# Optimization experiments

Measured on AMD Instinct MI355X. Metric: run time of the kernel, lower is better.

Reference implementation:

```python
import jax, jax.numpy as jnp
import numpy as np

TOP_K = 2

def setup_inputs() -> dict:
    key = jax.random.key(0)
    k1, k2, k3, k4 = jax.random.split(key, 4)
    B, T, C, E = 4, 2048, 1024, 8
    x = jax.random.normal(k1, (B, T, C), dtype=jnp.float32)
    Wg = jax.random.normal(k2, (C, E), dtype=jnp.float32) * 0.02
    W1 = jax.random.normal(k3, (E, C, 4 * C), dtype=jnp.float32) * 0.02
    W2 = jax.random.normal(k4, (E, 4 * C, C), dtype=jnp.float32) * 0.02
    return {"x": x, "Wg": Wg, "W1": W1, "W2": W2}

def reference(x, Wg, W1, W2):
    B, T, C = x.shape
    E = W1.shape[0]
    xf = x.reshape(-1, C)                                   # [N, C]
    N = xf.shape[0]
    gate = jax.nn.softmax(xf @ Wg, axis=-1)                 # [N, E]
    top_w, top_i = jax.lax.top_k(gate, TOP_K)               # [N, k]
    top_w = top_w / (top_w.sum(axis=-1, keepdims=True) + 1e-9)
    # Dense all-expert compute (equivalent math to gather/MLP/scatter loop)
    h = jnp.maximum(jnp.einsum('nc,ecf->nef', xf, W1), 0.0)  # [N, E, 4C]
    y = jnp.einsum('nef,efc->nec', h, W2)                    # [N, E, C]
    # Scatter top-k weights into a dense [N, E] combine matrix
    comb = jnp.zeros((N, E), dtype=xf.dtype).at[jnp.arange(N)[:, None], top_i].add(top_w)
    out = jnp.einsum('nec,ne->nc', y, comb)                  # [N, C]
    return out.reshape(B, T, C)
```

## Files before the change

kernel.cpp:

```cpp
#include <hip/hip_runtime.h>
#include <hip/hip_bf16.h>
#include <hip/hip_fp16.h>


#define N_TOK 8192
#define C_DIM 1024
#define F_DIM 4096
#define BM 128
#define M_BLOCKS 136
#define A_ROWS (M_BLOCKS*BM)

#define OFF_TOK  0u
#define OFF_WGT  69632u
#define OFF_MBLK 139264u
#define OFF_TE   140288u
#define OFF_TW   205824u
#define OFF_XB   271360u
#define OFF_WT   17048576u
#define OFF_H    84157440u

typedef __attribute__((ext_vector_type(8))) _Float16 f16x8;
typedef __attribute__((ext_vector_type(4))) float f32x4;
typedef __attribute__((ext_vector_type(8))) unsigned short u16x8;

__device__ __forceinline__ unsigned short f2h_bits(float x) {
    _Float16 h = (_Float16)x;
    return __builtin_bit_cast(unsigned short, h);
}

__device__ __forceinline__ void gload16(const void* g, void* l) {
    __builtin_amdgcn_global_load_lds(
        (const __attribute__((address_space(1))) unsigned int*)g,
        (__attribute__((address_space(3))) unsigned int*)l, 16, 0, 0);
}

__global__ __launch_bounds__(256) void gate_kernel(
    const float* __restrict__ x, const float* __restrict__ Wg,
    unsigned short* __restrict__ xb, int2* __restrict__ te, float2* __restrict__ tw)
{
    int w = threadIdx.x >> 6, lam = threadIdx.x & 63;
    int t = blockIdx.x * 4 + w;
    const float* xr = x + (size_t)t * C_DIM;
    unsigned short* xbr = xb + (size_t)t * C_DIM;
    float acc[8] = {0,0,0,0,0,0,0,0};
    for (int it = 0; it < C_DIM/64; ++it) {
        int c = it*64 + lam;
        float v = xr[c];
        xbr[c] = f2h_bits(v);
        const float4* wg = (const float4*)(Wg + c*8);
        float4 a = wg[0], b = wg[1];
        acc[0] += v*a.x; acc[1] += v*a.y; acc[2] += v*a.z; acc[3] += v*a.w;
        acc[4] += v*b.x; acc[5] += v*b.y; acc[6] += v*b.z; acc[7] += v*b.w;
    }
    #pragma unroll
    for (int off = 32; off > 0; off >>= 1)
        #pragma unroll
        for (int e = 0; e < 8; ++e)
            acc[e] += __shfl_xor(acc[e], off);
    if (lam == 0) {
        float m = acc[0];
        #pragma unroll
        for (int e = 1; e < 8; ++e) m = fmaxf(m, acc[e]);
        float ex[8], d = 0.f;
        #pragma unroll
        for (int e = 0; e < 8; ++e) { ex[e] = expf(acc[e] - m); d += ex[e]; }
        int e0 = 0;
        #pragma unroll
        for (int e = 1; e < 8; ++e) if (acc[e] > acc[e0]) e0 = e;
        int e1 = (e0 == 0) ? 1 : 0;
        #pragma unroll
        for (int e = 0; e < 8; ++e) if (e != e0 && acc[e] > acc[e1]) e1 = e;
        float g0 = ex[e0]/d, g1 = ex[e1]/d;
        float s = g0 + g1 + 1e-9f;
        te[t] = make_int2(e0, e1);
        tw[t] = make_float2(g0/s, g1/s);
    }
}

__global__ __launch_bounds__(1024) void route_kernel(
    const int2* __restrict__ te, const float2* __restrict__ tw,
    int* __restrict__ tok, float* __restrict__ wgt, int* __restrict__ mblk)
{
    __shared__ int cnt[8], curs[8], base[8], alen[8];
    int tid = threadIdx.x;
    if (tid < 8) { cnt[tid] = 0; curs[tid] = 0; }
    __syncthreads();
    for (int t = tid; t < N_TOK; t += 1024) {
        int2 ee = te[t];
        atomicAdd(&cnt[ee.x], 1); atomicAdd(&cnt[ee.y], 1);
    }
    __syncthreads();
    if (tid == 0) {
        int b = 0;
        for (int e = 0; e < 8; ++e) {
            base[e] = b;
            int a = ((cnt[e] + BM - 1) / BM) * BM;
            alen[e] = a;
            b += a;
        }
    }
    __syncthreads();
    for (int i = tid; i < A_ROWS; i += 1024) tok[i] = -1;
    for (int mb = tid; mb < M_BLOCKS; mb += 1024) {
        int r = mb * BM, ef = 0;
        for (int e = 0; e < 8; ++e)
            if (r >= base[e] && r < base[e] + alen[e]) ef = e;
        mblk[mb] = ef;
    }
    __syncthreads();
    for (int t = tid; t < N_TOK; t += 1024) {
        int2 ee = te[t]; float2 ww = tw[t];
        int p = atomicAdd(&curs[ee.x], 1);
        tok[base[ee.x] + p] = t; wgt[base[ee.x] + p] = ww.x;
        p = atomicAdd(&curs[ee.y], 1);
        tok[base[ee.y] + p] = t; wgt[base[ee.y] + p] = ww.y;
    }
}

__global__ __launch_bounds__(256) void transpose_kernel(
    const float* __restrict__ src, unsigned short* __restrict__ dst, int R, int Cd)
{
    __shared__ float tile[64][65];
    int tcN = Cd >> 6;
    int tilesPerE = (R >> 6) * tcN;
    int bid = blockIdx.x;
    int e = bid / tilesPerE;
    int tt = bid - e * tilesPerE;
    int tr = tt / tcN, tc = tt - tr * tcN;
    int R0 = tr << 6, C0 = tc << 6;
    const float* se = src + (size_t)e * R * Cd;
    unsigned short* de = dst + (size_t)e * R * Cd;
    int tid = threadIdx.x;
    int col4 = (tid & 15) << 2;
    int row0 = tid >> 4;
    #pragma unroll
    for (int j = 0; j < 4; ++j) {
        int row = row0 + j*16;
        float4 v = *(const float4*)(se + (size_t)(R0+row)*Cd + C0 + col4);
        tile[row][col4+0] = v.x; tile[row][col4+1] = v.y;
        tile[row][col4+2] = v.z; tile[row][col4+3] = v.w;
    }
    __syncthreads();
    int oc = tid >> 2;
    int og = tid & 3;
    u16x8 o0, o1;
    #pragma unroll
    for (int i = 0; i < 8; ++i) o0[i] = f2h_bits(tile[og*16 + i][oc]);
    #pragma unroll
    for (int i = 0; i < 8; ++i) o1[i] = f2h_bits(tile[og*16 + 8 + i][oc]);
    unsigned short* dp = de + (size_t)(C0+oc)*R + R0 + og*16;
    *(u16x8*)dp = o0;
    *(u16x8*)(dp + 8) = o1;
}

template<int K_DIM, int N_COLS, bool GATHER_A, bool RELU_H>
__global__ __launch_bounds__(256) void gemm_kernel(
    const unsigned short* __restrict__ Asrc, const unsigned short* __restrict__ Wt,
    const int* __restrict__ tok, const float* __restrict__ wgt,
    const int* __restrict__ mblk,
    unsigned short* __restrict__ hout, float* __restrict__ out)
{
    constexpr int KT = K_DIM / 32;
    __shared__ unsigned short As[BM*32];
    __shared__ unsigned short Bs[BM*32];
    int nb = blockIdx.x, mb = blockIdx.y;
    int e = mblk[mb];
    int aBase = mb*BM, nBase = nb*128;
    int tid = threadIdx.x, w = tid >> 6, lam = tid & 63;
    int wm = w >> 1, wn = w & 1;
    int rowInG = lam >> 2, cpr = lam & 3;

    const char* srcA[2]; const char* srcB[2];
    char* ldsA[2]; char* ldsB[2];
    #pragma unroll
    for (int i = 0; i < 2; ++i) {
        int g = w*2 + i;
        int ra = g*16 + rowInG;
        int cg = (cpr - (ra >> 1)) & 3;
        long arow;
        if (GATHER_A) { int tkn = tok[aBase + ra]; if (tkn < 0) tkn = 0; arow = tkn; }
        else          { arow = aBase + ra; }
        srcA[i] = (const char*)(Asrc + arow*(long)K_DIM) + cg*16;
        srcB[i] = (const char*)(Wt + ((long)e*N_COLS + nBase + ra)*(long)K_DIM) + cg*16;
        ldsA[i] = (char*)As + g*1024;
        ldsB[i] = (char*)Bs + g*1024;
    }

    const f32x4 z = {0.f, 0.f, 0.f, 0.f};
    f32x4 acc[4][4];
    #pragma unroll
    for (int mi = 0; mi < 4; ++mi)
        #pragma unroll
        for (int ni = 0; ni < 4; ++ni) acc[mi][ni] = z;

    for (int kt = 0; kt < KT; ++kt) {
        __syncthreads();
        long ko = (long)kt * 64;
        gload16(srcA[0] + ko, ldsA[0]);
        gload16(srcA[1] + ko, ldsA[1]);
        gload16(srcB[0] + ko, ldsB[0]);
        gload16(srcB[1] + ko, ldsB[1]);
        __syncthreads();

        f16x8 af[4], bf[4];
        #pragma unroll
        for (int mi = 0; mi < 4; ++mi) {
            int r = wm*64 + mi*16 + (lam & 15);
            int cs = ((lam >> 4) + (r >> 1)) & 3;
            af[mi] = *(const f16x8*)((const char*)As + r*64 + cs*16);
        }
        #pragma unroll
        for (int ni = 0; ni < 4; ++ni) {
            int r = wn*64 + ni*16 + (lam & 15);
            int cs = ((lam >> 4) + (r >> 1)) & 3;
            bf[ni] = *(const f16x8*)((const char*)Bs + r*64 + cs*16);
        }
        #pragma unroll
        for (int mi = 0; mi < 4; ++mi)
            #pragma unroll
            for (int ni = 0; ni < 4; ++ni)
                acc[mi][ni] = __builtin_amdgcn_mfma_f32_16x16x32_f16(af[mi], bf[ni], acc[mi][ni], 0, 0, 0);
    }

    #pragma unroll
    for (int mi = 0; mi < 4; ++mi) {
        int r0 = aBase + wm*64 + mi*16 + (lam >> 4)*4;
        #pragma unroll
        for (int ni = 0; ni < 4; ++ni) {
            int col = nBase + wn*64 + ni*16 + (lam & 15);
            f32x4 v = acc[mi][ni];
            if (RELU_H) {
                #pragma unroll
                for (int j = 0; j < 4; ++j)
                    hout[(size_t)(r0+j)*N_COLS + col] = f2h_bits(fmaxf(v[j], 0.f));
            } else {
                #pragma unroll
                for (int j = 0; j < 4; ++j) {
                    int ar = r0 + j;
                    int tkn = tok[ar];
                    if (tkn >= 0) atomicAdd(out + (size_t)tkn*C_DIM + col, wgt[ar]*v[j]);
                }
            }
        }
    }
}

extern "C" void kernel_launch(void* const* d_in, const int* in_sizes, int n_in,
                              void* d_out, int out_size, void* d_ws, size_t ws_size,
                              hipStream_t stream)
{
    const float* x  = (const float*)d_in[0];
    const float* Wg = (const float*)d_in[1];
    const float* W1 = (const float*)d_in[2];
    const float* W2 = (const float*)d_in[3];
    float* out = (float*)d_out;
    char* ws = (char*)d_ws;

    int*    tok  = (int*)(ws + OFF_TOK);
    float*  wgt  = (float*)(ws + OFF_WGT);
    int*    mblk = (int*)(ws + OFF_MBLK);
    int2*   te   = (int2*)(ws + OFF_TE);
    float2* tw   = (float2*)(ws + OFF_TW);
    unsigned short* xb = (unsigned short*)(ws + OFF_XB);
    unsigned short* wt = (unsigned short*)(ws + OFF_WT);
    unsigned short* h  = (unsigned short*)(ws + OFF_H);

    hipMemsetAsync(d_out, 0, (size_t)out_size * sizeof(float), stream);
    gate_kernel<<<N_TOK/4, 256, 0, stream>>>(x, Wg, xb, te, tw);
    route_kernel<<<1, 1024, 0, stream>>>(te, tw, tok, wgt, mblk);
    transpose_kernel<<<8192, 256, 0, stream>>>(W1, wt, 1024, 4096);
    gemm_kernel<1024, 4096, true,  true ><<<dim3(32, M_BLOCKS), 256, 0, stream>>>(xb, wt, tok, wgt, mblk, h, nullptr);
    transpose_kernel<<<8192, 256, 0, stream>>>(W2, wt, 4096, 1024);
    gemm_kernel<4096, 1024, false, false><<<dim3(8, M_BLOCKS), 256, 0, stream>>>(h, wt, tok, wgt, mblk, nullptr, out);
}
```

Baseline: 828.7 us.

## Use 256x256 tiles with 4-stage async LDS pipeline and XCD-aware block swizzle

Grows the grouped GEMM tile to 256x256 with 512 threads and switches from a single-buffered sync-load-sync loop to a 4-buffer ring, keeping two stages of global-to-LDS loads in flight under explicit vmcnt waits. Blocks are remapped so consecutive tiles land on the same XCD, and tiles whose first row is padding exit early. The goal is to hide load latency and raise arithmetic intensity per tile. In exchange, padding per expert grows with BM=256, LDS use is 128KB per block, and register pressure rises with 32 accumulators.

```diff
diff --git a/kernel.cpp b/kernel.cpp
--- a/kernel.cpp
+++ b/kernel.cpp
@@ -6,18 +6,18 @@
 #define N_TOK 8192
 #define C_DIM 1024
 #define F_DIM 4096
-#define BM 128
-#define M_BLOCKS 136
+#define BM 256
+#define M_BLOCKS 72
 #define A_ROWS (M_BLOCKS*BM)
 
 #define OFF_TOK  0u
-#define OFF_WGT  69632u
-#define OFF_MBLK 139264u
-#define OFF_TE   140288u
-#define OFF_TW   205824u
-#define OFF_XB   271360u
-#define OFF_WT   17048576u
-#define OFF_H    84157440u
+#define OFF_WGT  73728u
+#define OFF_MBLK 147456u
+#define OFF_TE   148480u
+#define OFF_TW   214016u
+#define OFF_XB   279552u
+#define OFF_WT   17056768u
+#define OFF_H    84165632u
 
 typedef __attribute__((ext_vector_type(8))) _Float16 f16x8;
 typedef __attribute__((ext_vector_type(4))) float f32x4;
@@ -154,92 +154,122 @@
 }
 
 template<int K_DIM, int N_COLS, bool GATHER_A, bool RELU_H>
-__global__ __launch_bounds__(256) void gemm_kernel(
+__global__ __launch_bounds__(512, 2) void gemm_kernel(
     const unsigned short* __restrict__ Asrc, const unsigned short* __restrict__ Wt,
     const int* __restrict__ tok, const float* __restrict__ wgt,
     const int* __restrict__ mblk,
     unsigned short* __restrict__ hout, float* __restrict__ out)
 {
     constexpr int KT = K_DIM / 32;
-    __shared__ unsigned short As[BM*32];
-    __shared__ unsigned short Bs[BM*32];
-    int nb = blockIdx.x, mb = blockIdx.y;
+    constexpr int NB = N_COLS / 256;
+    __shared__ _Float16 As[4][256*32];
+    __shared__ _Float16 Bs[4][256*32];
+
+    constexpr int nwg = NB * M_BLOCKS;
+    constexpr int cpx = nwg >> 3;
+    int bid = blockIdx.x;
+    int wg = (bid & 7) * cpx + (bid >> 3);
+    int nb = wg % NB;
+    int mb = wg / NB;
+    int aBase = mb * BM, nBase = nb * 256;
+    if (tok[aBase] < 0) return;
     int e = mblk[mb];
-    int aBase = mb*BM, nBase = nb*128;
+
     int tid = threadIdx.x, w = tid >> 6, lam = tid & 63;
-    int wm = w >> 1, wn = w & 1;
-    int rowInG = lam >> 2, cpr = lam & 3;
-
-    const char* srcA[2]; const char* srcB[2];
-    char* ldsA[2]; char* ldsB[2];
+    int wm = w >> 2, wn = w & 3;
+
+    int rl = lam >> 2;
+    int cg = ((lam & 3) - ((lam >> 3) & 3)) & 3;
+    const char* gA[2]; const char* gB[2];
     #pragma unroll
     for (int i = 0; i < 2; ++i) {
-        int g = w*2 + i;
-        int ra = g*16 + rowInG;
-        int cg = (cpr - (ra >> 1)) & 3;
+        int s = w*2 + i;
+        int tr = s*16 + rl;
         long arow;
-        if (GATHER_A) { int tkn = tok[aBase + ra]; if (tkn < 0) tkn = 0; arow = tkn; }
-        else          { arow = aBase + ra; }
-        srcA[i] = (const char*)(Asrc + arow*(long)K_DIM) + cg*16;
-        srcB[i] = (const char*)(Wt + ((long)e*N_COLS + nBase + ra)*(long)K_DIM) + cg*16;
-        ldsA[i] = (char*)As + g*1024;
-        ldsB[i] = (char*)Bs + g*1024;
-    }
+        if (GATHER_A) { int tk = tok[aBase + tr]; if (tk < 0) tk = 0; arow = tk; }
+        else          { arow = aBase + tr; }
+        gA[i] = (const char*)(Asrc + arow*(long)K_DIM) + cg*16;
+        gB[i] = (const char*)(Wt + ((long)e*N_COLS + nBase + tr)*(long)K_DIM) + cg*16;
+    }
+
+    auto STAGE = [&](int t) {
+        int b = t & 3;
+        long ko = (long)t * 64;
+        gload16(gA[0] + ko, (char*)&As[b][0] + (w*2+0)*1024);
+        gload16(gA[1] + ko, (char*)&As[b][0] + (w*2+1)*1024);
+        gload16(gB[0] + ko, (char*)&Bs[b][0] + (w*2+0)*1024);
+        gload16(gB[1] + ko, (char*)&Bs[b][0] + (w*2+1)*1024);
+    };
+
+    int slot = ((lam >> 4) + (((lam & 15)) >> 1)) & 3;
+    int rA = wm*128 + (lam & 15);
+    int rB = wn*64 + (lam & 15);
+    int offA = rA*64 + slot*16;
+    int offB = rB*64 + slot*16;
 
     const f32x4 z = {0.f, 0.f, 0.f, 0.f};
-    f32x4 acc[4][4];
-    #pragma unroll
-    for (int mi = 0; mi < 4; ++mi)
+    f32x4 acc[8][4];
+    #pragma unroll
+    for (int mi = 0; mi < 8; ++mi)
         #pragma unroll
         for (int ni = 0; ni < 4; ++ni) acc[mi][ni] = z;
 
-    for (int kt = 0; kt < KT; ++kt) {
-        __syncthreads();
-        long ko = (long)kt * 64;
-        gload16(srcA[0] + ko, ldsA[0]);
-        gload16(srcA[1] + ko, ldsA[1]);
-        gload16(srcB[0] + ko, ldsB[0]);
-        gload16(srcB[1] + ko, ldsB[1]);
-        __syncthreads();
-
-        f16x8 af[4], bf[4];
-        #pragma unroll
-        for (int mi = 0; mi < 4; ++mi) {
-            int r = wm*64 + mi*16 + (lam & 15);
-            int cs = ((lam >> 4) + (r >> 1)) & 3;
-            af[mi] = *(const f16x8*)((const char*)As + r*64 + cs*16);
-        }
-        #pragma unroll
-        for (int ni = 0; ni < 4; ++ni) {
-            int r = wn*64 + ni*16 + (lam & 15);
-            int cs = ((lam >> 4) + (r >> 1)) & 3;
-            bf[ni] = *(const f16x8*)((const char*)Bs + r*64 + cs*16);
-        }
-        #pragma unroll
-        for (int mi = 0; mi < 4; ++mi)
+    STAGE(0); STAGE(1);
+    for (int j = 0; j < KT; ++j) {
+        if (j + 2 < KT) {
+            STAGE(j + 2);
+            asm volatile("s_waitcnt vmcnt(8)" ::: "memory");
+        } else if (j + 1 < KT) {
+            asm volatile("s_waitcnt vmcnt(4)" ::: "memory");
+        } else {
+            asm volatile("s_waitcnt vmcnt(0)" ::: "memory");
+        }
+        __builtin_amdgcn_s_barrier();
+        __builtin_amdgcn_sched_barrier(0);
+        asm volatile("" ::: "memory");
+        const char* Ab = (const char*)&As[j & 3][0];
+        const char* Bb = (const char*)&Bs[j & 3][0];
+        f16x8 bf[4];
+        #pragma unroll
+        for (int ni = 0; ni < 4; ++ni)
+            bf[ni] = *(const f16x8*)(Bb + offB + ni*1024);
+        #pragma unroll
+        for (int mi = 0; mi < 8; ++mi) {
+            f16x8 af = *(const f16x8*)(Ab + offA + mi*1024);
             #pragma unroll
             for (int ni = 0; ni < 4; ++ni)
-                acc[mi][ni] = __builtin_amdgcn_mfma_f32_16x16x32_f16(af[mi], bf[ni], acc[mi][ni], 0, 0, 0);
-    }
-
-    #pragma unroll
-    for (int mi = 0; mi < 4; ++mi) {
-        int r0 = aBase + wm*64 + mi*16 + (lam >> 4)*4;
-        #pragma unroll
-        for (int ni = 0; ni < 4; ++ni) {
-            int col = nBase + wn*64 + ni*16 + (lam & 15);
-            f32x4 v = acc[mi][ni];
-            if (RELU_H) {
+                acc[mi][ni] = __builtin_amdgcn_mfma_f32_16x16x32_f16(af, bf[ni], acc[mi][ni], 0, 0, 0);
+        }
+    }
+
+    int orow = (lam >> 4) * 4;
+    int ocol = lam & 15;
+    if (RELU_H) {
+        #pragma unroll
+        for (int mi = 0; mi < 8; ++mi) {
+            size_t r0 = (size_t)aBase + wm*128 + mi*16 + orow;
+            #pragma unroll
+            for (int ni = 0; ni < 4; ++ni) {
+                int col = nBase + wn*64 + ni*16 + ocol;
+                f32x4 v = acc[mi][ni];
                 #pragma unroll
-                for (int j = 0; j < 4; ++j)
-                    hout[(size_t)(r0+j)*N_COLS + col] = f2h_bits(fmaxf(v[j], 0.f));
-            } else {
+                for (int jj = 0; jj < 4; ++jj)
+                    hout[(r0+jj)*(size_t)N_COLS + col] = f2h_bits(fmaxf(v[jj], 0.f));
+            }
+        }
+    } else {
+        #pragma unroll
+        for (int mi = 0; mi < 8; ++mi) {
+            int r0 = aBase + wm*128 + mi*16 + orow;
+            #pragma unroll
+            for (int jj = 0; jj < 4; ++jj) {
+                int tk = tok[r0 + jj];
+                if (tk < 0) continue;
+                float wv = wgt[r0 + jj];
+                float* op = out + (size_t)tk * C_DIM + nBase + wn*64 + ocol;
                 #pragma unroll
-                for (int j = 0; j < 4; ++j) {
-                    int ar = r0 + j;
-                    int tkn = tok[ar];
-                    if (tkn >= 0) atomicAdd(out + (size_t)tkn*C_DIM + col, wgt[ar]*v[j]);
-                }
+                for (int ni = 0; ni < 4; ++ni)
+                    atomicAdd(op + ni*16, wv * acc[mi][ni][jj]);
             }
         }
     }
@@ -269,7 +299,7 @@
     gate_kernel<<<N_TOK/4, 256, 0, stream>>>(x, Wg, xb, te, tw);
     route_kernel<<<1, 1024, 0, stream>>>(te, tw, tok, wgt, mblk);
     transpose_kernel<<<8192, 256, 0, stream>>>(W1, wt, 1024, 4096);
-    gemm_kernel<1024, 4096, true,  true ><<<dim3(32, M_BLOCKS), 256, 0, stream>>>(xb, wt, tok, wgt, mblk, h, nullptr);
+    gemm_kernel<1024, 4096, true,  true ><<<16*M_BLOCKS, 512, 0, stream>>>(xb, wt, tok, wgt, mblk, h, nullptr);
     transpose_kernel<<<8192, 256, 0, stream>>>(W2, wt, 4096, 1024);
-    gemm_kernel<4096, 1024, false, false><<<dim3(8, M_BLOCKS), 256, 0, stream>>>(h, wt, tok, wgt, mblk, nullptr, out);
-}
+    gemm_kernel<4096, 1024, false, false><<<4*M_BLOCKS, 512, 0, stream>>>(h, wt, tok, wgt, mblk, nullptr, out);
+}
```

After: 851.8 us. 1.03x slower.
